# Performance work log

Measured on AMD Instinct MI355X. Metric: run time of the kernel, lower is better.

The kernel has to match this reference:

```python
import jax, jax.numpy as jnp
import numpy as np

DT = 0.01
MAXLAG = 3.0
NLAG = int(MAXLAG / DT)   # same float->int math as the torch module
NMA = 20


def setup_inputs() -> dict:
    key = jax.random.key(0)
    k1, k2, k3, k4 = jax.random.split(key, 4)
    B, C, F = 32, 128, 2049  # F = nfast/2 + 1, nfast = 4096
    data1 = jax.random.normal(k1, (B, C, F, 2), dtype=jnp.float32)
    data2 = jax.random.normal(k2, (B, C, F, 2), dtype=jnp.float32)
    event1 = jax.random.randint(k3, (B,), 0, 100000, dtype=jnp.int64 if jax.config.jax_enable_x64 else jnp.int32)
    event2 = jax.random.randint(k4, (B,), 0, 100000, dtype=jnp.int64 if jax.config.jax_enable_x64 else jnp.int32)
    return {"data1": data1, "data2": data2, "event1": event1, "event2": event2}


def reference(data1, data2, event1, event2):
    # view_as_complex: trailing dim 2 = (re, im)
    c1 = jax.lax.complex(data1[..., 0], data1[..., 1])  # [B, C, F]
    c2 = jax.lax.complex(data2[..., 0], data2[..., 1])
    F = c1.shape[-1]
    nfast = (F - 1) * 2

    # cross-spectrum and inverse rFFT (channel_shift == 0)
    xf = jnp.conj(c1) * c2
    xt = jnp.fft.irfft(xf, n=nfast, axis=-1)          # [B, C, nfast]
    xt = jnp.roll(xt, nfast // 2, axis=-1)
    xcor = xt[..., nfast // 2 - NLAG + 1: nfast // 2 + NLAG]  # [B, C, T], T = 2*NLAG-1

    # AvgPool1d(NMA, stride=1, padding=NMA//2) over the CHANNEL axis (dim 1),
    # count_include_pad=True -> windowed zero-padded sum divided by NMA, keep first C rows
    pad = NMA // 2
    C = xcor.shape[1]
    wsum = jax.lax.reduce_window(
        xcor, 0.0, jax.lax.add,
        window_dimensions=(1, NMA, 1), window_strides=(1, 1, 1),
        padding=[(0, 0), (pad, pad), (0, 0)])          # [B, C+1, T]
    xcor = (wsum / NMA)[:, :C, :]                      # [B, C, T]

    # peak pick: pick max, but swap in min where |min| > max
    vmax = jnp.max(xcor, axis=-1)
    imax = jnp.argmax(xcor, axis=-1)
    vmin = jnp.min(xcor, axis=-1)
    imin = jnp.argmin(xcor, axis=-1)
    ineg = jnp.abs(vmin) > vmax
    cc = jnp.where(ineg, vmin, vmax)                   # [B, C]
    idx = jnp.where(ineg, imin, imax)
    tshift = (idx - NLAG + 1).astype(jnp.float32) * DT # [B, C]
    return (cc, tshift, event1, event2)
```

## Files before the change

### kernel.cpp

```cpp
#include <hip/hip_runtime.h>
#include <math.h>

#define NBINS 2049
#define NXC   599
#define LST   640
#define TWO_PI 6.283185307179586f

#define CPAD(c) ((c) + 2 * ((c) >> 6))

struct cpx { float r, i; };
__device__ inline cpx cmul(cpx a, cpx b) { return cpx{a.r * b.r - a.i * b.i, a.r * b.i + a.i * b.r}; }

__device__ inline void dft4i(float& r0, float& i0, float& r1, float& i1,
                             float& r2, float& i2, float& r3, float& i3) {
    float t0r = r0 + r2, t0i = i0 + i2;
    float t1r = r0 - r2, t1i = i0 - i2;
    float t2r = r1 + r3, t2i = i1 + i3;
    float t3r = r1 - r3, t3i = i1 - i3;
    r0 = t0r + t2r; i0 = t0i + t2i;
    r2 = t0r - t2r; i2 = t0i - t2i;
    r1 = t1r - t3i; i1 = t1i + t3r;
    r3 = t1r + t3i; i3 = t1i - t3r;
}

__device__ inline void radix8_bfly(float r[8], float im[8]) {
    float er0 = r[0], ei0 = im[0], er1 = r[2], ei1 = im[2];
    float er2 = r[4], ei2 = im[4], er3 = r[6], ei3 = im[6];
    float or0 = r[1], oi0 = im[1], or1 = r[3], oi1 = im[3];
    float or2 = r[5], oi2 = im[5], or3 = r[7], oi3 = im[7];
    dft4i(er0, ei0, er1, ei1, er2, ei2, er3, ei3);
    dft4i(or0, oi0, or1, oi1, or2, oi2, or3, oi3);
    const float C = 0.70710678118654752f;
    float w1r = C * (or1 - oi1), w1i = C * (or1 + oi1);
    float w2r = -oi2,            w2i = or2;
    float w3r = -C * (or3 + oi3), w3i = C * (or3 - oi3);
    r[0] = er0 + or0; im[0] = ei0 + oi0;
    r[4] = er0 - or0; im[4] = ei0 - oi0;
    r[1] = er1 + w1r; im[1] = ei1 + w1i;
    r[5] = er1 - w1r; im[5] = ei1 - w1i;
    r[2] = er2 + w2r; im[2] = ei2 + w2i;
    r[6] = er2 - w2r; im[6] = ei2 - w2i;
    r[3] = er3 + w3r; im[3] = ei3 + w3i;
    r[7] = er3 - w3r; im[7] = ei3 - w3i;
}

__device__ inline void dft16i(float xr[16], float xi[16]) {
    float er[8], ei[8], odr[8], odi[8];
#pragma unroll
    for (int k = 0; k < 8; ++k) {
        er[k] = xr[2 * k];      ei[k] = xi[2 * k];
        odr[k] = xr[2 * k + 1]; odi[k] = xi[2 * k + 1];
    }
    radix8_bfly(er, ei);
    radix8_bfly(odr, odi);
    const float c1 = 0.92387953251128675613f;
    const float s1 = 0.38268343236508977173f;
    const float C  = 0.70710678118654752440f;
    float tr[8], td[8];
    tr[0] = odr[0];                      td[0] = odi[0];
    tr[1] = c1 * odr[1] - s1 * odi[1];   td[1] = c1 * odi[1] + s1 * odr[1];
    tr[2] = C * (odr[2] - odi[2]);       td[2] = C * (odr[2] + odi[2]);
    tr[3] = s1 * odr[3] - c1 * odi[3];   td[3] = s1 * odi[3] + c1 * odr[3];
    tr[4] = -odi[4];                     td[4] = odr[4];
    tr[5] = -s1 * odr[5] - c1 * odi[5];  td[5] = -s1 * odi[5] + c1 * odr[5];
    tr[6] = -C * (odr[6] + odi[6]);      td[6] = C * (odr[6] - odi[6]);
    tr[7] = -c1 * odr[7] - s1 * odi[7];  td[7] = -c1 * odi[7] + s1 * odr[7];
#pragma unroll
    for (int k = 0; k < 8; ++k) {
        xr[k]     = er[k] + tr[k];  xi[k]     = ei[k] + td[k];
        xr[k + 8] = er[k] - tr[k];  xi[k + 8] = ei[k] - td[k];
    }
}

__device__ inline void apply_tw15(float zr[16], float zi[16], float cs, float sn) {
    cpx w[16];
    w[1]  = cpx{cs, sn};
    w[2]  = cmul(w[1], w[1]);
    w[3]  = cmul(w[1], w[2]);
    w[4]  = cmul(w[2], w[2]);
    w[5]  = cmul(w[2], w[3]);
    w[6]  = cmul(w[3], w[3]);
    w[7]  = cmul(w[3], w[4]);
    w[8]  = cmul(w[4], w[4]);
    w[9]  = cmul(w[4], w[5]);
    w[10] = cmul(w[5], w[5]);
    w[11] = cmul(w[5], w[6]);
    w[12] = cmul(w[6], w[6]);
    w[13] = cmul(w[6], w[7]);
    w[14] = cmul(w[7], w[7]);
    w[15] = cmul(w[7], w[8]);
#pragma unroll
    for (int k = 1; k < 16; ++k) {
        float a = zr[k] * w[k].r - zi[k] * w[k].i;
        float b = zr[k] * w[k].i + zi[k] * w[k].r;
        zr[k] = a; zi[k] = b;
    }
}

__global__ __launch_bounds__(128, 4) void k1_fft(const float2* __restrict__ d1,
                                                 const float2* __restrict__ d2,
                                                 float* __restrict__ ws) {
    __shared__ float2 S[2113];
    const int row = blockIdx.x;
    const int tt = threadIdx.x;
    const float2* p1 = d1 + (long)row * NBINS;
    const float2* p2 = d2 + (long)row * NBINS;

    float xr_[16], xi_[16];
#pragma unroll
    for (int j = 0; j < 16; ++j) {
        int c = tt + 128 * j;
        float2 a = p1[c], bb = p2[c];
        xr_[j] = a.x * bb.x + a.y * bb.y;
        xi_[j] = a.x * bb.y - a.y * bb.x;
        S[CPAD(c)] = make_float2(xr_[j], xi_[j]);
    }
    if (tt == 127) {
        float2 a = p1[2048], bb = p2[2048];
        S[2112] = make_float2(a.x * bb.x + a.y * bb.y, 0.0f);
    }
    if (tt == 0) xi_[0] = 0.0f;
    __syncthreads();

    const float WC[16] = { 1.0f, 0.98078528040323044913f, 0.92387953251128675613f,
        0.83146961230254523708f, 0.70710678118654752440f, 0.55557023301960222474f,
        0.38268343236508977173f, 0.19509032201612826785f, 0.0f,
        -0.19509032201612826785f, -0.38268343236508977173f, -0.55557023301960222474f,
        -0.70710678118654752440f, -0.83146961230254523708f, -0.92387953251128675613f,
        -0.98078528040323044913f };
    const float WS[16] = { 0.0f, 0.19509032201612826785f, 0.38268343236508977173f,
        0.55557023301960222474f, 0.70710678118654752440f, 0.83146961230254523708f,
        0.92387953251128675613f, 0.98078528040323044913f, 1.0f,
        0.98078528040323044913f, 0.92387953251128675613f, 0.83146961230254523708f,
        0.70710678118654752440f, 0.55557023301960222474f, 0.38268343236508977173f,
        0.19509032201612826785f };
    float zr[16], zi[16];
    float sn, cs;
    __sincosf((float)tt * (TWO_PI / 4096.0f), &sn, &cs);
    const float h = 2.44140625e-4f;
#pragma unroll
    for (int j = 0; j < 16; ++j) {
        float2 m = S[CPAD(2048 - tt - 128 * j)];
        float er = h * (xr_[j] + m.x), ei = h * (xi_[j] - m.y);
        float dr = h * (xr_[j] - m.x), di = h * (xi_[j] + m.y);
        float twr = cs * WC[j] - sn * WS[j];
        float twi = cs * WS[j] + sn * WC[j];
        zr[j] = er - twi * dr - twr * di;
        zi[j] = ei + twr * dr - twi * di;
    }

    dft16i(zr, zi);
    __sincosf((float)tt * (TWO_PI / 2048.0f), &sn, &cs);
    apply_tw15(zr, zi, cs, sn);
    __syncthreads();
#pragma unroll
    for (int k = 0; k < 16; ++k)
        S[CPAD(tt + 128 * k)] = make_float2(zr[k], zi[k]);
    __syncthreads();

    const int s2 = tt >> 3, i2 = tt & 7;
    const int base2 = 128 * s2 + i2;
#pragma unroll
    for (int j = 0; j < 16; ++j) {
        float2 v = S[CPAD(base2 + 8 * j)];
        zr[j] = v.x; zi[j] = v.y;
    }
    dft16i(zr, zi);
    __sincosf((float)i2 * (TWO_PI / 128.0f), &sn, &cs);
    apply_tw15(zr, zi, cs, sn);
#pragma unroll
    for (int k = 0; k < 16; ++k)
        S[CPAD(base2 + 8 * k)] = make_float2(zr[k], zi[k]);
    __syncthreads();

    float ar[8], ai[8], br[8], bi[8];
#pragma unroll
    for (int r = 0; r < 4; ++r) {
        float4 v = *(const float4*)&S[CPAD(16 * tt + 2 * r)];
        ar[2 * r] = v.x; ai[2 * r] = v.y; ar[2 * r + 1] = v.z; ai[2 * r + 1] = v.w;
    }
#pragma unroll
    for (int r = 0; r < 4; ++r) {
        float4 v = *(const float4*)&S[CPAD(16 * tt + 8 + 2 * r)];
        br[2 * r] = v.x; bi[2 * r] = v.y; br[2 * r + 1] = v.z; bi[2 * r + 1] = v.w;
    }
    radix8_bfly(ar, ai);
    radix8_bfly(br, bi);

    float* wrow = ws + (long)row * LST;
    {
        int sb = 2 * tt;
        int m0 = (sb >> 4) + 16 * (sb & 15);
        if (m0 <= 149) { wrow[2 * m0 + 299] = ar[0]; wrow[2 * m0 + 300] = ai[0]; }
        if (m0 >= 107)      { wrow[2 * m0 - 213] = ar[7]; wrow[2 * m0 - 212] = ai[7]; }
        else if (m0 == 106) { wrow[0] = ai[7]; }
    }
    {
        int sb = 2 * tt + 1;
        int m0 = (sb >> 4) + 16 * (sb & 15);
        if (m0 <= 149) { wrow[2 * m0 + 299] = br[0]; wrow[2 * m0 + 300] = bi[0]; }
        if (m0 >= 107)      { wrow[2 * m0 - 213] = br[7]; wrow[2 * m0 - 212] = bi[7]; }
        else if (m0 == 106) { wrow[0] = bi[7]; }
    }
}

__global__ __launch_bounds__(128) void k2a_prefix(float* __restrict__ ws) {
    const int b = blockIdx.x / 5;
    const int l = (blockIdx.x % 5) * 128 + threadIdx.x;
    if (l >= NXC) return;
    float* base = ws + (long)b * 128 * LST + l;
    float run = 0.0f;
#pragma unroll 4
    for (int c = 0; c < 128; ++c) {
        run += base[c * LST];
        base[c * LST] = run;
    }
}

__global__ __launch_bounds__(128) void k2b_pick(const float* __restrict__ ws,
                                                const int* __restrict__ e1,
                                                const int* __restrict__ e2,
                                                float* __restrict__ out) {
    const int bc = blockIdx.x;
    const int b = bc >> 7, c = bc & 127;
    const int t = threadIdx.x;
    const float* Pb = ws + (long)(b * 128) * LST;
    const float* hi = Pb + (long)min(c + 9, 127) * LST;
    const bool has_lo = (c >= 11);
    const float* lo = Pb + (long)(has_lo ? (c - 11) : 0) * LST;

    float vmax = -3.0e38f; int imax = 0;
    float vmin = 3.0e38f;  int imin = 0;
    for (int l = t; l < NXC; l += 128) {
        float s = hi[l] - (has_lo ? lo[l] : 0.0f);
        s *= (1.0f / 20.0f);
        if (s > vmax) { vmax = s; imax = l; }
        if (s < vmin) { vmin = s; imin = l; }
    }

    __shared__ float smax[128], smin[128];
    __shared__ int   sxi[128], sni[128];
    smax[t] = vmax; sxi[t] = imax; smin[t] = vmin; sni[t] = imin;
    __syncthreads();
    for (int off = 64; off > 0; off >>= 1) {
        if (t < off) {
            float v2 = smax[t + off]; int i2 = sxi[t + off];
            if (v2 > smax[t] || (v2 == smax[t] && i2 < sxi[t])) { smax[t] = v2; sxi[t] = i2; }
            float u2 = smin[t + off]; int j2 = sni[t + off];
            if (u2 < smin[t] || (u2 == smin[t] && j2 < sni[t])) { smin[t] = u2; sni[t] = j2; }
        }
        __syncthreads();
    }
    if (t == 0) {
        float vx = smax[0], vn = smin[0];
        int ix = sxi[0], in_ = sni[0];
        bool ineg = fabsf(vn) > vx;
        float ccv = ineg ? vn : vx;
        int idx = ineg ? in_ : ix;
        out[bc] = ccv;
        out[4096 + bc] = (float)(idx - 299) * 0.01f;
    }
    if (bc == 0 && t < 32) out[8192 + t] = (float)e1[t];
    if (bc == 1 && t < 32) out[8224 + t] = (float)e2[t];
}

extern "C" void kernel_launch(void* const* d_in, const int* in_sizes, int n_in,
                              void* d_out, int out_size, void* d_ws, size_t ws_size,
                              hipStream_t stream) {
    const float2* d1 = (const float2*)d_in[0];
    const float2* d2 = (const float2*)d_in[1];
    const int* e1 = (const int*)d_in[2];
    const int* e2 = (const int*)d_in[3];
    float* out = (float*)d_out;
    float* ws = (float*)d_ws;

    k1_fft<<<dim3(4096), dim3(128), 0, stream>>>(d1, d2, ws);
    k2a_prefix<<<dim3(160), dim3(128), 0, stream>>>(ws);
    k2b_pick<<<dim3(4096), dim3(128), 0, stream>>>(ws, e1, e2, out);
}
```

Baseline: 50.16 us.

## Process two rows per FFT block, prefetching second row during first FFT

Each k1_fft block now handles two consecutive rows. The second row's inputs are loaded into registers before the first row's FFT runs, so their global-memory latency overlaps with the FFT compute. The 1/4096 scale factor moves into the cross-spectrum computation, and the grid is halved. The extra 64 live floats per thread raise register pressure under the launch bound of 4 blocks/SM and may cause spills or lower occupancy.

```diff
diff --git a/kernel.cpp b/kernel.cpp
--- a/kernel.cpp
+++ b/kernel.cpp
@@ -97,31 +97,9 @@
     }
 }
 
-__global__ __launch_bounds__(128, 4) void k1_fft(const float2* __restrict__ d1,
-                                                 const float2* __restrict__ d2,
-                                                 float* __restrict__ ws) {
-    __shared__ float2 S[2113];
-    const int row = blockIdx.x;
-    const int tt = threadIdx.x;
-    const float2* p1 = d1 + (long)row * NBINS;
-    const float2* p2 = d2 + (long)row * NBINS;
-
-    float xr_[16], xi_[16];
-#pragma unroll
-    for (int j = 0; j < 16; ++j) {
-        int c = tt + 128 * j;
-        float2 a = p1[c], bb = p2[c];
-        xr_[j] = a.x * bb.x + a.y * bb.y;
-        xi_[j] = a.x * bb.y - a.y * bb.x;
-        S[CPAD(c)] = make_float2(xr_[j], xi_[j]);
-    }
-    if (tt == 127) {
-        float2 a = p1[2048], bb = p2[2048];
-        S[2112] = make_float2(a.x * bb.x + a.y * bb.y, 0.0f);
-    }
-    if (tt == 0) xi_[0] = 0.0f;
-    __syncthreads();
-
+__device__ inline void fft_row(const float xr_[16], const float xi_[16],
+                               float2* __restrict__ S, int tt,
+                               float* __restrict__ wrow) {
     const float WC[16] = { 1.0f, 0.98078528040323044913f, 0.92387953251128675613f,
         0.83146961230254523708f, 0.70710678118654752440f, 0.55557023301960222474f,
         0.38268343236508977173f, 0.19509032201612826785f, 0.0f,
@@ -136,13 +114,13 @@
         0.19509032201612826785f };
     float zr[16], zi[16];
     float sn, cs;
+
     __sincosf((float)tt * (TWO_PI / 4096.0f), &sn, &cs);
-    const float h = 2.44140625e-4f;
 #pragma unroll
     for (int j = 0; j < 16; ++j) {
         float2 m = S[CPAD(2048 - tt - 128 * j)];
-        float er = h * (xr_[j] + m.x), ei = h * (xi_[j] - m.y);
-        float dr = h * (xr_[j] - m.x), di = h * (xi_[j] + m.y);
+        float er = xr_[j] + m.x, ei = xi_[j] - m.y;
+        float dr = xr_[j] - m.x, di = xi_[j] + m.y;
         float twr = cs * WC[j] - sn * WS[j];
         float twi = cs * WS[j] + sn * WC[j];
         zr[j] = er - twi * dr - twr * di;
@@ -187,7 +165,6 @@
     radix8_bfly(ar, ai);
     radix8_bfly(br, bi);
 
-    float* wrow = ws + (long)row * LST;
     {
         int sb = 2 * tt;
         int m0 = (sb >> 4) + 16 * (sb & 15);
@@ -202,6 +179,63 @@
         if (m0 >= 107)      { wrow[2 * m0 - 213] = br[7]; wrow[2 * m0 - 212] = bi[7]; }
         else if (m0 == 106) { wrow[0] = bi[7]; }
     }
+}
+
+__global__ __launch_bounds__(128, 4) void k1_fft(const float2* __restrict__ d1,
+                                                 const float2* __restrict__ d2,
+                                                 float* __restrict__ ws) {
+    __shared__ float2 S[2113];
+    const int tt = threadIdx.x;
+    const int row0 = blockIdx.x << 1;
+    const float h = 2.44140625e-4f;
+
+    const float2* p1 = d1 + (long)row0 * NBINS;
+    const float2* p2 = d2 + (long)row0 * NBINS;
+    const float2* q1 = p1 + NBINS;
+    const float2* q2 = p2 + NBINS;
+
+    float x0r[16], x0i[16];
+#pragma unroll
+    for (int j = 0; j < 16; ++j) {
+        int c = tt + 128 * j;
+        float2 a = p1[c], bb = p2[c];
+        x0r[j] = h * (a.x * bb.x + a.y * bb.y);
+        x0i[j] = h * (a.x * bb.y - a.y * bb.x);
+        if (c == 0) x0i[j] = 0.0f;
+        S[CPAD(c)] = make_float2(x0r[j], x0i[j]);
+    }
+    if (tt == 127) {
+        float2 a = p1[2048], bb = p2[2048];
+        S[2112] = make_float2(h * (a.x * bb.x + a.y * bb.y), 0.0f);
+    }
+
+    float2 a1[16], b1[16], ny1, ny2;
+#pragma unroll
+    for (int j = 0; j < 16; ++j) {
+        int c = tt + 128 * j;
+        a1[j] = q1[c];
+        b1[j] = q2[c];
+    }
+    if (tt == 127) { ny1 = q1[2048]; ny2 = q2[2048]; }
+
+    __syncthreads();
+    fft_row(x0r, x0i, S, tt, ws + (long)row0 * LST);
+    __syncthreads();
+
+    float x1r[16], x1i[16];
+#pragma unroll
+    for (int j = 0; j < 16; ++j) {
+        int c = tt + 128 * j;
+        x1r[j] = h * (a1[j].x * b1[j].x + a1[j].y * b1[j].y);
+        x1i[j] = h * (a1[j].x * b1[j].y - a1[j].y * b1[j].x);
+        if (c == 0) x1i[j] = 0.0f;
+        S[CPAD(c)] = make_float2(x1r[j], x1i[j]);
+    }
+    if (tt == 127) {
+        S[2112] = make_float2(h * (ny1.x * ny2.x + ny1.y * ny2.y), 0.0f);
+    }
+    __syncthreads();
+    fft_row(x1r, x1i, S, tt, ws + (long)(row0 + 1) * LST);
 }
 
 __global__ __launch_bounds__(128) void k2a_prefix(float* __restrict__ ws) {
@@ -274,7 +308,7 @@
     float* out = (float*)d_out;
     float* ws = (float*)d_ws;
 
-    k1_fft<<<dim3(4096), dim3(128), 0, stream>>>(d1, d2, ws);
+    k1_fft<<<dim3(2048), dim3(128), 0, stream>>>(d1, d2, ws);
     k2a_prefix<<<dim3(160), dim3(128), 0, stream>>>(ws);
     k2b_pick<<<dim3(4096), dim3(128), 0, stream>>>(ws, e1, e2, out);
 }
```

Measured after the change: 167.6 us. +234.1%, slower.
